# Kernel optimization log

Hardware: AMD Instinct MI355X
Metric: run time of the kernel (lower is better)

Reference implementation:

```python
import jax, jax.numpy as jnp
import numpy as np

V, DM, IMG, H, M = 32000, 256, 512, 256, 16
B, K, L, T = 16, 32, 32, 128

def setup_inputs():
    key = jax.random.key(0)
    ks = jax.random.split(key, 22)
    s = 0.02
    p = lambda i, shape: jax.random.normal(ks[i], shape, jnp.float32) * s
    return {
        "ctx_input_ids": jax.random.randint(ks[0], (B, K, L), 0, V),
        "ctx_attn_mask": jnp.ones((B, K, L), jnp.int32),
        "ctx_img_emb": jax.random.normal(ks[1], (B, K, IMG), jnp.float32),
        "tgt_input_ids": jax.random.randint(ks[2], (B, T), 0, V),
        "emb_text": p(3, (V, DM)),
        "Wih_t": p(4, (3 * DM, DM)), "Whh_t": p(5, (3 * DM, DM)),
        "bih_t": p(6, (3 * DM,)), "bhh_t": p(7, (3 * DM,)),
        "fuse_W": p(8, (H, DM + IMG)), "fuse_b": p(9, (H,)),
        "mem_init": p(10, (M, H)),
        "Wih_c": p(11, (3 * H, H)), "Whh_c": p(12, (3 * H, H)),
        "bih_c": p(13, (3 * H,)), "bhh_c": p(14, (3 * H,)),
        "tok_emb": p(15, (V, H)),
        "Wih_d": p(16, (3 * H, H)), "Whh_d": p(17, (3 * H, H)),
        "bih_d": p(18, (3 * H,)), "bhh_d": p(19, (3 * H,)),
        "head_W": p(20, (V, H)), "head_b": p(21, (V,)),
    }

def _gru(x, h0, Wih, Whh, bih, bhh, mask=None):
    # x: (B, S, I) -> outs (B, S, Hd), hN (B, Hd). PyTorch GRU equations.
    xg = jnp.einsum('bti,gi->btg', x, Wih) + bih  # precompute input-side gates (B,S,3H)
    if mask is None:
        mask = jnp.ones(x.shape[:2], bool)
    def step(h, inp):
        xt, mt = inp  # (B,3H), (B,)
        hg = h @ Whh.T + bhh
        xr, xz, xn = jnp.split(xt, 3, -1)
        hr, hz, hn = jnp.split(hg, 3, -1)
        r = jax.nn.sigmoid(xr + hr)
        z = jax.nn.sigmoid(xz + hz)
        n = jnp.tanh(xn + r * hn)
        h_new = (1.0 - z) * n + z * h
        h = jnp.where(mt[:, None], h_new, h)  # hold state on padded steps
        return h, h
    hN, outs = jax.lax.scan(step, h0, (jnp.moveaxis(xg, 1, 0), jnp.moveaxis(mask, 1, 0)))
    return jnp.moveaxis(outs, 0, 1), hN

def _forward(ctx_input_ids, ctx_attn_mask, ctx_img_emb, tgt_input_ids,
             emb_text, Wih_t, Whh_t, bih_t, bhh_t, fuse_W, fuse_b, mem_init,
             Wih_c, Whh_c, bih_c, bhh_c, tok_emb, Wih_d, Whh_d, bih_d, bhh_d,
             head_W, head_b):
    b, k, l = ctx_input_ids.shape
    dm = emb_text.shape[1]
    h = fuse_W.shape[0]
    # FrameTextEncoder: embedding + masked GRU, final hidden per frame
    tok = emb_text[ctx_input_ids.reshape(b * k, l)]  # (BK, L, DM)
    mask = ctx_attn_mask.reshape(b * k, l).astype(bool)
    _, tvec = _gru(tok, jnp.zeros((b * k, dm), tok.dtype), Wih_t, Whh_t, bih_t, bhh_t, mask)
    tvec = tvec.reshape(b, k, dm)
    # Fuse text + image
    z = jnp.tanh(jnp.concatenate([tvec, ctx_img_emb], -1) @ fuse_W.T + fuse_b)  # (B,K,H)
    # Memory slot loop over K frames (sequential softmax read then erase/add write)
    mem0 = jnp.broadcast_to(mem_init, (b,) + mem_init.shape)
    inv_sqrt_d = 1.0 / float(np.sqrt(h))
    def mem_step(mem, q):
        w = jax.nn.softmax(jnp.einsum('bmd,bd->bm', mem, q) * inv_sqrt_d, -1)
        readout = jnp.einsum('bm,bmd->bd', w, mem)
        mem = mem * (1.0 - w[..., None]) + w[..., None] * q[:, None, :]
        return mem, q + readout
    _, z_mem = jax.lax.scan(mem_step, mem0, jnp.moveaxis(z, 1, 0))
    z2 = jnp.moveaxis(z_mem, 0, 1)  # (B, K, H)
    _, h0 = _gru(z2, jnp.zeros((b, h), z2.dtype), Wih_c, Whh_c, bih_c, bhh_c)
    # Decoder over target tokens (teacher forcing)
    x = tok_emb[tgt_input_ids[:, :-1]]  # (B, T-1, H)
    outs, _ = _gru(x, h0, Wih_d, Whh_d, bih_d, bhh_d)
    return outs @ head_W.T + head_b  # (B, T-1, V)

def reference(ctx_input_ids, ctx_attn_mask, ctx_img_emb, tgt_input_ids,
              emb_text, Wih_t, Whh_t, bih_t, bhh_t, fuse_W, fuse_b, mem_init,
              Wih_c, Whh_c, bih_c, bhh_c, tok_emb, Wih_d, Whh_d, bih_d, bhh_d,
              head_W, head_b):
    return _forward(ctx_input_ids, ctx_attn_mask, ctx_img_emb, tgt_input_ids,
                    emb_text, Wih_t, Whh_t, bih_t, bhh_t, fuse_W, fuse_b, mem_init,
                    Wih_c, Whh_c, bih_c, bhh_c, tok_emb, Wih_d, Whh_d, bih_d, bhh_d,
                    head_W, head_b)
```

## Files before the change

kernel.cpp:

```cpp
#include <hip/hip_runtime.h>
#include <hip/hip_bf16.h>

typedef __attribute__((ext_vector_type(4))) float f32x4;
typedef __attribute__((ext_vector_type(8))) short short8;
typedef __attribute__((ext_vector_type(4))) unsigned int u32x4;
typedef __attribute__((ext_vector_type(4))) unsigned short u16x4;

static __device__ __forceinline__ unsigned short f2bf(float f){
  unsigned u = __builtin_bit_cast(unsigned, f);
  u += 0x7FFFu + ((u >> 16) & 1u);
  return (unsigned short)(u >> 16);
}
static __device__ __forceinline__ float bf2f(unsigned short b){
  return __builtin_bit_cast(float, ((unsigned)b) << 16);
}
static __device__ __forceinline__ unsigned char f2e4m3(float x){
  unsigned u = __builtin_bit_cast(unsigned, x);
  unsigned s = (u >> 24) & 0x80u;
  float ax = __builtin_fabsf(x);
  if (ax < 0.015625f) {
    int q = (int)(ax * 512.f + 0.5f);
    return (unsigned char)(s | (unsigned)q);
  }
  if (ax > 448.f) return (unsigned char)(s | 0x7Eu);
  unsigned v = __builtin_bit_cast(unsigned, ax);
  v += 0x00080000u + ((v >> 20) & 1u);
  if (__builtin_bit_cast(float, v & 0xFFF00000u) > 448.f)
    return (unsigned char)(s | 0x7Eu);
  unsigned ee = ((v >> 23) & 0xFFu) - 127u + 7u;
  unsigned m = (v >> 20) & 7u;
  return (unsigned char)(s | (ee << 3) | m);
}
static __device__ __forceinline__ unsigned char h2fp8(float hx16){
#if __has_builtin(__builtin_amdgcn_cvt_pk_fp8_f32)
  int pk = __builtin_amdgcn_cvt_pk_fp8_f32(hx16, hx16, 0, false);
  return (unsigned char)(pk & 0xFF);
#else
  return f2e4m3(hx16);
#endif
}
static __device__ __forceinline__ f32x4 mfma16(short8 a, short8 b, f32x4 c){
  return __builtin_amdgcn_mfma_f32_16x16x32_bf16(a, b, c, 0, 0, 0);
}
static __device__ __forceinline__ f32x4 mfma8(long a, long b, f32x4 c){
  return __builtin_amdgcn_mfma_f32_16x16x32_fp8_fp8(a, b, c, 0, 0, 0);
}
static __device__ __forceinline__ float rcpf(float x){ return __builtin_amdgcn_rcpf(x); }
static __device__ __forceinline__ float sigf(float x){ return rcpf(1.f + __expf(-x)); }
static __device__ __forceinline__ float tanhfast(float x){
  float e = __expf(2.f*x);
  return (e - 1.f) * rcpf(e + 1.f);
}

__global__ __launch_bounds__(256) void k_cvt(
    const float* __restrict__ sh, unsigned short* __restrict__ dh,
    const float* __restrict__ s0, const float* __restrict__ s1,
    const float* __restrict__ s2, const float* __restrict__ s3,
    const float* __restrict__ s4, const float* __restrict__ s5,
    const float* __restrict__ s6,
    unsigned short* __restrict__ d0, unsigned short* __restrict__ d1,
    unsigned short* __restrict__ d2, unsigned short* __restrict__ d3,
    unsigned short* __restrict__ d4, unsigned short* __restrict__ d5,
    unsigned short* __restrict__ d6)
{
  const long NH4 = 2048000;
  const long NS4 = 49152;
  const long total = NH4 + 7*NS4;
  for (long idx = (long)blockIdx.x*blockDim.x + threadIdx.x; idx < total;
       idx += (long)gridDim.x*blockDim.x) {
    const float* s; unsigned short* d; long off;
    if (idx < NH4) { s = sh; d = dh; off = idx; }
    else {
      long r = idx - NH4; int mat = (int)(r / NS4); off = r - (long)mat*NS4;
      switch (mat) {
        case 0: s=s0; d=d0; break;  case 1: s=s1; d=d1; break;
        case 2: s=s2; d=d2; break;  case 3: s=s3; d=d3; break;
        case 4: s=s4; d=d4; break;  case 5: s=s5; d=d5; break;
        default: s=s6; d=d6; break;
      }
    }
    f32x4 v = ((const f32x4*)s)[off];
    u16x4 o2;
    o2[0]=f2bf(v[0]); o2[1]=f2bf(v[1]); o2[2]=f2bf(v[2]); o2[3]=f2bf(v[3]);
    ((u16x4*)d)[off] = o2;
  }
}

__global__ __launch_bounds__(256) void k_cvtw(
    const float* __restrict__ s0, const float* __restrict__ s1,
    const float* __restrict__ s2,
    unsigned short* __restrict__ r0, unsigned short* __restrict__ r1,
    unsigned short* __restrict__ r2,
    unsigned char* __restrict__ z0, unsigned char* __restrict__ z1,
    unsigned char* __restrict__ z2)
{
  int idx = blockIdx.x*256 + threadIdx.x;
  if (idx >= 3*24576) return;
  int mat = idx / 24576, c = idx % 24576;
  const float* s = (mat==0) ? s0 : (mat==1 ? s1 : s2);
  if (c < 8192) {
    unsigned short* d = (mat==0) ? r0 : (mat==1 ? r1 : r2);
    int w = c >> 9, rest = c & 511;
    int kb = rest >> 6, lane = rest & 63;
    int row = w*16 + (lane & 15);
    int k0  = kb*32 + (lane >> 4)*8;
    const float* sp = s + (long)row*256 + k0;
    f32x4 a = *(const f32x4*)sp;
    f32x4 b = *(const f32x4*)(sp + 4);
    short8 o;
    o[0]=(short)f2bf(a[0]); o[1]=(short)f2bf(a[1]);
    o[2]=(short)f2bf(a[2]); o[3]=(short)f2bf(a[3]);
    o[4]=(short)f2bf(b[0]); o[5]=(short)f2bf(b[1]);
    o[6]=(short)f2bf(b[2]); o[7]=(short)f2bf(b[3]);
    *(short8*)(d + (long)c*8) = o;
  } else {
    int c2 = c - 8192;
    unsigned char* d = (mat==0) ? z0 : (mat==1 ? z1 : z2);
    int w = c2 >> 10, rest = c2 & 1023;
    int g = rest >> 9, r_ = rest & 511;
    int kb = r_ >> 6, lane = r_ & 63;
    int row = (1+g)*256 + w*16 + (lane & 15);
    int k0  = kb*32 + (lane >> 4)*8;
    const float* sp = s + (long)row*256 + k0;
    f32x4 a = *(const f32x4*)sp;
    f32x4 b = *(const f32x4*)(sp + 4);
    unsigned char ob[8];
    ob[0]=f2e4m3(a[0]*16.f); ob[1]=f2e4m3(a[1]*16.f);
    ob[2]=f2e4m3(a[2]*16.f); ob[3]=f2e4m3(a[3]*16.f);
    ob[4]=f2e4m3(b[0]*16.f); ob[5]=f2e4m3(b[1]*16.f);
    ob[6]=f2e4m3(b[2]*16.f); ob[7]=f2e4m3(b[3]*16.f);
    unsigned lo = (unsigned)ob[0] | ((unsigned)ob[1]<<8) |
                  ((unsigned)ob[2]<<16) | ((unsigned)ob[3]<<24);
    unsigned hi = (unsigned)ob[4] | ((unsigned)ob[5]<<8) |
                  ((unsigned)ob[6]<<16) | ((unsigned)ob[7]<<24);
    *(unsigned*)(d + (long)c2*8)     = lo;
    *(unsigned*)(d + (long)c2*8 + 4) = hi;
  }
}

template<int TN, int TS, int EPI>
__global__ __launch_bounds__(256) void k_gemm(
    const float* __restrict__ tabA, int ldA,
    const float* __restrict__ tabB2, int ldB2, int K1,
    const int* __restrict__ ids,
    const unsigned short* __restrict__ W,
    const float* __restrict__ bias,
    int M, int Ktot,
    void* __restrict__ outp, int ldOut)
{
  const int bm = blockIdx.x, bn = blockIdx.y;
  const int tid = threadIdx.x;
  const int lane = tid & 63, w = tid >> 6;
  const int l15 = lane & 15, l4 = lane >> 4;

  const int r_g = bm*64 + w*16 + l15;
  const int r_c = (r_g < M) ? r_g : (M-1);
  long row_src;
  if (ids) { int ii = (r_c / TN) * TS + (r_c % TN); row_src = ids[ii]; }
  else row_src = r_c;

  const int kchunk = l4 * 8;
  const int ncol0 = bn*128 + l15;

  f32x4 acc[8];
  #pragma unroll
  for (int i=0;i<8;i++){ f32x4 z4 = {0.f,0.f,0.f,0.f}; acc[i]=z4; }

  const int KB = Ktot >> 5;
  for (int kb = 0; kb < KB; ++kb) {
    int k = kb*32 + kchunk;
    const float* ap;
    if (tabB2 && k >= K1) ap = tabB2 + row_src*(long)ldB2 + (k - K1);
    else                  ap = tabA  + row_src*(long)ldA  + k;
    f32x4 a0 = *(const f32x4*)ap;
    f32x4 a1 = *(const f32x4*)(ap + 4);
    short8 afr;
    afr[0]=(short)f2bf(a0[0]); afr[1]=(short)f2bf(a0[1]);
    afr[2]=(short)f2bf(a0[2]); afr[3]=(short)f2bf(a0[3]);
    afr[4]=(short)f2bf(a1[0]); afr[5]=(short)f2bf(a1[1]);
    afr[6]=(short)f2bf(a1[2]); afr[7]=(short)f2bf(a1[3]);
    #pragma unroll
    for (int ct=0; ct<8; ++ct) {
      int n = ncol0 + ct*16;
      short8 bfr = *(const short8*)(W + (long)n*Ktot + k);
      acc[ct] = mfma16(afr, bfr, acc[ct]);
    }
  }

  #pragma unroll
  for (int ct=0; ct<8; ++ct) {
    int n = ncol0 + ct*16;
    float bv = bias[n];
    #pragma unroll
    for (int q=0; q<4; ++q) {
      int rr = bm*64 + w*16 + l4*4 + q;
      if (rr < M) {
        float v = acc[ct][q] + bv;
        if (EPI == 1) ((float*)outp)[(long)rr*ldOut + n] = tanhfast(v);
        else ((unsigned short*)outp)[(long)rr*ldOut + n] = f2bf(v);
      }
    }
  }
}

__global__ __launch_bounds__(1024, 1) void k_gru(
    const unsigned short* __restrict__ WR,
    const unsigned char*  __restrict__ WZN,
    const float* __restrict__ bhh,
    const unsigned short* __restrict__ xg,
    const int* __restrict__ mask,
    const unsigned short* __restrict__ h0bf,
    float* __restrict__ hNf,
    unsigned short* __restrict__ hNbf,
    unsigned short* __restrict__ outs,
    int T)
{
  __shared__ unsigned char  Wzn[131072];
  __shared__ unsigned short hbz[9*264];
  __shared__ unsigned char  h8z[9*264];
  __shared__ float          hg[4][776];

  const int tid = threadIdx.x;
  const int w = tid >> 6, lane = tid & 63;
  const int l15 = lane & 15, l4 = lane >> 4;
  const int rowbase = blockIdx.x * 4;
  const int uw = w*16 + l15;
  const int gr = tid >> 8;
  const int gu = tid & 255;

  #pragma unroll
  for (int i=0; i<8; ++i) {
    int c = i*1024 + tid;
    *(u32x4*)&Wzn[(long)c*16] = *(const u32x4*)(WZN + (long)c*16);
  }

  short8 Br[8];
  #pragma unroll
  for (int kb=0; kb<8; ++kb)
    Br[kb] = *(const short8*)(WR + ((long)(w*8+kb)*512) + lane*8);

  const float b_r = bhh[gu], b_z = bhh[256+gu], b_n = bhh[512+gu];

  const int arow0 = (l15 < 4) ? l15     : 8;
  const int arow1 = (l15 < 4) ? 4 + l15 : 8;
  const int hbO0 = (arow0*264 + l4*8)*2;
  const int hbO1 = (arow1*264 + l4*8)*2;
  const int h8O0 =  arow0*264 + l4*8;
  const int h8O1 =  arow1*264 + l4*8;

  if (tid < 264) { hbz[8*264 + tid] = 0; h8z[8*264 + tid] = 0; }
  float h = h0bf ? bf2f(h0bf[(rowbase+gr)*256 + gu]) : 0.f;
  hbz[gr*264 + gu] = f2bf(h);
  h8z[gr*264 + gu] = h2fp8(h * 16.f);
  __syncthreads();

  const float inv256 = 0.00390625f;

  for (int t=0; t<T; ++t) {
    const int p = t & 1;

    const long xrow = (long)(rowbase + gr)*T + t;
    const unsigned short* xp = xg + xrow*768;
    const unsigned short xr_ = xp[gu];
    const unsigned short xz_ = xp[256+gu];
    const unsigned short xn_ = xp[512+gu];
    const int mok = mask ? mask[xrow] : 1;

    const int hbO = p ? hbO1 : hbO0;
    const int h8O = p ? h8O1 : h8O0;
    f32x4 aR={0.f,0.f,0.f,0.f}, aZ={0.f,0.f,0.f,0.f}, aN={0.f,0.f,0.f,0.f};
    #pragma unroll
    for (int kb=0; kb<8; ++kb) {
      short8 af = *(const short8*)((const char*)hbz + hbO + kb*64);
      long   a8 = *(const long*)((const char*)h8z + h8O + kb*32);
      aR = mfma16(af, Br[kb], aR);
      aZ = mfma8(a8, *(const long*)&Wzn[((long)((w*2+0)*8+kb)*512) + lane*8], aZ);
      aN = mfma8(a8, *(const long*)&Wzn[((long)((w*2+1)*8+kb)*512) + lane*8], aN);
    }
    if (l4 == 0) {
      #pragma unroll
      for (int q=0; q<4; ++q) {
        hg[q][uw]       = aR[q];
        hg[q][256+uw]   = aZ[q];
        hg[q][512+uw]   = aN[q];
      }
    }
    __syncthreads();

    float rr = sigf(bf2f(xr_) + hg[gr][gu] + b_r);
    float zz = sigf(bf2f(xz_) + hg[gr][256+gu]*inv256 + b_z);
    float nn = tanhfast(bf2f(xn_) + rr*(hg[gr][512+gu]*inv256 + b_n));
    float hv = nn + zz*(h - nn);
    if (!mok) hv = h;
    h = hv;
    const int wrow = (p^1)*4 + gr;
    const unsigned short hbv = f2bf(hv);
    hbz[wrow*264 + gu] = hbv;
    h8z[wrow*264 + gu] = h2fp8(hv * 16.f);
    if (outs) outs[xrow*256 + gu] = hbv;
    __syncthreads();
  }

  if (hNf)  hNf[(long)(rowbase+gr)*256 + gu] = h;
  if (hNbf) hNbf[(rowbase+gr)*256 + gu] = f2bf(h);
}

__global__ __launch_bounds__(64) void k_mem(
    const float* __restrict__ z,
    const float* __restrict__ mem_init,
    float* __restrict__ z2)
{
  const int b = blockIdx.x;
  const int lane = threadIdx.x;
  float mem[16][4];
  #pragma unroll
  for (int m=0; m<16; ++m) {
    f32x4 v = *(const f32x4*)(mem_init + m*256 + lane*4);
    mem[m][0]=v[0]; mem[m][1]=v[1]; mem[m][2]=v[2]; mem[m][3]=v[3];
  }
  for (int t=0; t<32; ++t) {
    f32x4 q = *(const f32x4*)(z + ((long)b*32 + t)*256 + lane*4);
    float s[16];
    #pragma unroll
    for (int m=0; m<16; ++m)
      s[m] = mem[m][0]*q[0] + mem[m][1]*q[1] + mem[m][2]*q[2] + mem[m][3]*q[3];
    #pragma unroll
    for (int st=1; st<64; st<<=1) {
      #pragma unroll
      for (int m=0; m<16; ++m) s[m] += __shfl_xor(s[m], st, 64);
    }
    float mx = -1e30f;
    #pragma unroll
    for (int m=0; m<16; ++m) { s[m] *= 0.0625f; mx = fmaxf(mx, s[m]); }
    float sum = 0.f;
    #pragma unroll
    for (int m=0; m<16; ++m) { s[m] = __expf(s[m]-mx); sum += s[m]; }
    float inv = rcpf(sum);
    f32x4 ro = {0.f,0.f,0.f,0.f};
    #pragma unroll
    for (int m=0; m<16; ++m) {
      float wm = s[m]*inv;
      #pragma unroll
      for (int c=0; c<4; ++c) {
        ro[c] += wm * mem[m][c];
        mem[m][c] += wm * (q[c] - mem[m][c]);
      }
    }
    f32x4 o = q + ro;
    *(f32x4*)(z2 + ((long)b*32 + t)*256 + lane*4) = o;
  }
}

__global__ __launch_bounds__(256) void k_head(
    const unsigned short* __restrict__ A,
    const unsigned short* __restrict__ Bw,
    const float* __restrict__ bias,
    float* __restrict__ out,
    int M)
{
  __shared__ unsigned short Bs[32768];
  const int bid = blockIdx.x;
  const int mt = bid % 16, nt = bid / 16;
  const int tid = threadIdx.x;
  const int lane = tid & 63, w = tid >> 6;
  const int l15 = lane & 15, l4 = lane >> 4;

  const long nbase = (long)nt * 128;
  #pragma unroll
  for (int it=0; it<16; ++it) {
    int idx = it*256 + tid;
    int rr = idx >> 5;
    int ch = idx & 31;
    int sch = ch ^ (rr & 7);
    u32x4 v = *(const u32x4*)(Bw + (nbase+rr)*256 + sch*8);
    *(u32x4*)&Bs[(long)idx*8] = v;
  }
  __syncthreads();

  const int m0 = mt*128 + w*32;
  const int arow0 = m0 + l15, arow1 = arow0 + 16;
  const int kc = l4 * 8;

  f32x4 acc[2][8];
  #pragma unroll
  for (int rt=0; rt<2; ++rt)
    #pragma unroll
    for (int ct=0; ct<8; ++ct){ f32x4 z4={0.f,0.f,0.f,0.f}; acc[rt][ct]=z4; }

  #pragma unroll
  for (int kb=0; kb<8; ++kb) {
    short8 a0 = *(const short8*)(A + (long)arow0*256 + kb*32 + kc);
    short8 a1 = *(const short8*)(A + (long)arow1*256 + kb*32 + kc);
    int c = kb*4 + l4;
    #pragma unroll
    for (int ct=0; ct<8; ++ct) {
      int n_local = ct*16 + l15;
      int sc = c ^ (n_local & 7);
      short8 bf = *(const short8*)&Bs[((long)n_local*32 + sc)*8];
      acc[0][ct] = mfma16(a0, bf, acc[0][ct]);
      acc[1][ct] = mfma16(a1, bf, acc[1][ct]);
    }
  }

  #pragma unroll
  for (int ct=0; ct<8; ++ct) {
    int n_g = nt*128 + ct*16 + l15;
    float bv = bias[n_g];
    #pragma unroll
    for (int rt=0; rt<2; ++rt) {
      #pragma unroll
      for (int q=0; q<4; ++q) {
        int r_g = m0 + rt*16 + l4*4 + q;
        if (r_g < M) out[(long)r_g*32000 + n_g] = acc[rt][ct][q] + bv;
      }
    }
  }
}

extern "C" void kernel_launch(void* const* d_in, const int* in_sizes, int n_in,
                              void* d_out, int out_size, void* d_ws, size_t ws_size,
                              hipStream_t stream)
{
  (void)in_sizes; (void)n_in; (void)out_size; (void)ws_size;
  const int*   ctx_ids  = (const int*)  d_in[0];
  const int*   ctx_mask = (const int*)  d_in[1];
  const float* img      = (const float*)d_in[2];
  const int*   tgt_ids  = (const int*)  d_in[3];
  const float* emb_text = (const float*)d_in[4];
  const float* Wih_t    = (const float*)d_in[5];
  const float* Whh_t    = (const float*)d_in[6];
  const float* bih_t    = (const float*)d_in[7];
  const float* bhh_t    = (const float*)d_in[8];
  const float* fuse_W   = (const float*)d_in[9];
  const float* fuse_b   = (const float*)d_in[10];
  const float* mem_init = (const float*)d_in[11];
  const float* Wih_c    = (const float*)d_in[12];
  const float* Whh_c    = (const float*)d_in[13];
  const float* bih_c    = (const float*)d_in[14];
  const float* bhh_c    = (const float*)d_in[15];
  const float* tok_emb  = (const float*)d_in[16];
  const float* Wih_d    = (const float*)d_in[17];
  const float* Whh_d    = (const float*)d_in[18];
  const float* bih_d    = (const float*)d_in[19];
  const float* bhh_d    = (const float*)d_in[20];
  const float* head_W   = (const float*)d_in[21];
  const float* head_b   = (const float*)d_in[22];
  float* out = (float*)d_out;
  char* ws = (char*)d_ws;

  size_t o = 0;
  auto alloc = [&](size_t bytes){ size_t r = o; o += (bytes + 255) & ~(size_t)255; return r; };
  unsigned short* wWih_t = (unsigned short*)(ws + alloc(768*256*2));
  unsigned short* wWhh_t = (unsigned short*)(ws + alloc(768*256*2));
  unsigned short* wWih_c = (unsigned short*)(ws + alloc(768*256*2));
  unsigned short* wWhh_c = (unsigned short*)(ws + alloc(768*256*2));
  unsigned short* wWih_d = (unsigned short*)(ws + alloc(768*256*2));
  unsigned short* wWhh_d = (unsigned short*)(ws + alloc(768*256*2));
  unsigned short* wFuse  = (unsigned short*)(ws + alloc(256*768*2));
  unsigned short* wR_t   = (unsigned short*)(ws + alloc(65536*2));
  unsigned short* wR_c   = (unsigned short*)(ws + alloc(65536*2));
  unsigned short* wR_d   = (unsigned short*)(ws + alloc(65536*2));
  unsigned char*  wZN_t  = (unsigned char*)(ws + alloc(131072));
  unsigned char*  wZN_c  = (unsigned char*)(ws + alloc(131072));
  unsigned char*  wZN_d  = (unsigned char*)(ws + alloc(131072));
  unsigned short* wHead  = (unsigned short*)(ws + alloc((size_t)32000*256*2));
  unsigned short* xg_t   = (unsigned short*)(ws + alloc((size_t)16384*768*2));
  unsigned short* xg_c   = (unsigned short*)(ws + alloc((size_t)512*768*2));
  unsigned short* xg_d   = (unsigned short*)(ws + alloc((size_t)2032*768*2));
  float*          tvec   = (float*)(ws + alloc((size_t)512*256*4));
  float*          zbuf   = (float*)(ws + alloc((size_t)512*256*4));
  float*          z2buf  = (float*)(ws + alloc((size_t)512*256*4));
  unsigned short* outsb  = (unsigned short*)(ws + alloc((size_t)2048*256*2));
  unsigned short* hbdec  = (unsigned short*)(ws + alloc((size_t)16*256*2));

  k_cvt<<<2048, 256, 0, stream>>>(head_W, wHead,
      Wih_t, Whh_t, Wih_c, Whh_c, Wih_d, Whh_d, fuse_W,
      wWih_t, wWhh_t, wWih_c, wWhh_c, wWih_d, wWhh_d, wFuse);
  k_cvtw<<<288, 256, 0, stream>>>(Whh_t, Whh_c, Whh_d,
                                  wR_t, wR_c, wR_d, wZN_t, wZN_c, wZN_d);

  k_gemm<32,32,0><<<dim3(256,6), 256, 0, stream>>>(
      emb_text, 256, nullptr, 0, 256, ctx_ids, wWih_t, bih_t, 16384, 256, xg_t, 768);

  k_gemm<127,128,0><<<dim3(32,6), 256, 0, stream>>>(
      tok_emb, 256, nullptr, 0, 256, tgt_ids, wWih_d, bih_d, 2032, 256, xg_d, 768);

  k_gru<<<128, 1024, 0, stream>>>(wR_t, wZN_t, bhh_t, xg_t, ctx_mask,
                                  nullptr, tvec, nullptr, nullptr, 32);

  k_gemm<1,1,1><<<dim3(8,2), 256, 0, stream>>>(
      tvec, 256, img, 512, 256, nullptr, wFuse, fuse_b, 512, 768, zbuf, 256);

  k_mem<<<16, 64, 0, stream>>>(zbuf, mem_init, z2buf);

  k_gemm<1,1,0><<<dim3(8,6), 256, 0, stream>>>(
      z2buf, 256, nullptr, 0, 256, nullptr, wWih_c, bih_c, 512, 256, xg_c, 768);

  k_gru<<<4, 1024, 0, stream>>>(wR_c, wZN_c, bhh_c, xg_c, nullptr,
                                nullptr, nullptr, hbdec, nullptr, 32);

  k_gru<<<4, 1024, 0, stream>>>(wR_d, wZN_d, bhh_d, xg_d, nullptr,
                                hbdec, nullptr, nullptr, outsb, 127);

  k_head<<<4000, 256, 0, stream>>>(outsb, wHead, head_b, out, 2032);
}
```

Baseline: 728.0 us.

## Keep GRU recurrent weights in registers and redistribute gates via shuffles

The GRU step kernel no longer stages the fp8 z/n recurrent weights in shared memory; each wave keeps its slice in registers. The hidden-gate results are redistributed from the MFMA accumulator layout to per-thread units with wave shuffles instead of a shared-memory scratch buffer, which removes one block-wide barrier per timestep. Thread-to-(row,unit) mapping changes so each lane's gate values match its shuffled accumulator entries. This raises register pressure per thread and adds shuffle instructions in exchange for fewer barriers and less LDS traffic on the serial recurrence.

```diff
diff --git a/kernel.cpp b/kernel.cpp
--- a/kernel.cpp
+++ b/kernel.cpp
@@ -50,6 +50,15 @@
 static __device__ __forceinline__ float tanhfast(float x){
   float e = __expf(2.f*x);
   return (e - 1.f) * rcpf(e + 1.f);
+}
+static __device__ __forceinline__ float spread4(f32x4 v, int l15, int l4){
+  float x0 = __shfl(v[0], l15, 64);
+  float x1 = __shfl(v[1], l15, 64);
+  float x2 = __shfl(v[2], l15, 64);
+  float x3 = __shfl(v[3], l15, 64);
+  float s01 = (l4 & 1) ? x1 : x0;
+  float s23 = (l4 & 1) ? x3 : x2;
+  return (l4 & 2) ? s23 : s01;
 }
 
 __global__ __launch_bounds__(256) void k_cvt(
@@ -215,31 +224,26 @@
     unsigned short* __restrict__ outs,
     int T)
 {
-  __shared__ unsigned char  Wzn[131072];
   __shared__ unsigned short hbz[9*264];
   __shared__ unsigned char  h8z[9*264];
-  __shared__ float          hg[4][776];
 
   const int tid = threadIdx.x;
   const int w = tid >> 6, lane = tid & 63;
   const int l15 = lane & 15, l4 = lane >> 4;
   const int rowbase = blockIdx.x * 4;
-  const int uw = w*16 + l15;
-  const int gr = tid >> 8;
-  const int gu = tid & 255;
-
-  #pragma unroll
-  for (int i=0; i<8; ++i) {
-    int c = i*1024 + tid;
-    *(u32x4*)&Wzn[(long)c*16] = *(const u32x4*)(WZN + (long)c*16);
-  }
+  const int u = w*16 + l15;
+  const int gr = l4;
 
   short8 Br[8];
-  #pragma unroll
-  for (int kb=0; kb<8; ++kb)
-    Br[kb] = *(const short8*)(WR + ((long)(w*8+kb)*512) + lane*8);
-
-  const float b_r = bhh[gu], b_z = bhh[256+gu], b_n = bhh[512+gu];
+  long Bz8[8], Bn8[8];
+  #pragma unroll
+  for (int kb=0; kb<8; ++kb) {
+    Br[kb]  = *(const short8*)(WR + ((long)(w*8+kb)*512) + lane*8);
+    Bz8[kb] = *(const long*)(WZN + ((long)((w*2+0)*8+kb)*512) + lane*8);
+    Bn8[kb] = *(const long*)(WZN + ((long)((w*2+1)*8+kb)*512) + lane*8);
+  }
+
+  const float b_r = bhh[u], b_z = bhh[256+u], b_n = bhh[512+u];
 
   const int arow0 = (l15 < 4) ? l15     : 8;
   const int arow1 = (l15 < 4) ? 4 + l15 : 8;
@@ -249,9 +253,9 @@
   const int h8O1 =  arow1*264 + l4*8;
 
   if (tid < 264) { hbz[8*264 + tid] = 0; h8z[8*264 + tid] = 0; }
-  float h = h0bf ? bf2f(h0bf[(rowbase+gr)*256 + gu]) : 0.f;
-  hbz[gr*264 + gu] = f2bf(h);
-  h8z[gr*264 + gu] = h2fp8(h * 16.f);
+  float h = h0bf ? bf2f(h0bf[(rowbase+gr)*256 + u]) : 0.f;
+  hbz[gr*264 + u] = f2bf(h);
+  h8z[gr*264 + u] = h2fp8(h * 16.f);
   __syncthreads();
 
   const float inv256 = 0.00390625f;
@@ -261,9 +265,9 @@
 
     const long xrow = (long)(rowbase + gr)*T + t;
     const unsigned short* xp = xg + xrow*768;
-    const unsigned short xr_ = xp[gu];
-    const unsigned short xz_ = xp[256+gu];
-    const unsigned short xn_ = xp[512+gu];
+    const unsigned short xr_ = xp[u];
+    const unsigned short xz_ = xp[256+u];
+    const unsigned short xn_ = xp[512+u];
     const int mok = mask ? mask[xrow] : 1;
 
     const int hbO = p ? hbO1 : hbO0;
@@ -274,35 +278,30 @@
       short8 af = *(const short8*)((const char*)hbz + hbO + kb*64);
       long   a8 = *(const long*)((const char*)h8z + h8O + kb*32);
       aR = mfma16(af, Br[kb], aR);
-      aZ = mfma8(a8, *(const long*)&Wzn[((long)((w*2+0)*8+kb)*512) + lane*8], aZ);
-      aN = mfma8(a8, *(const long*)&Wzn[((long)((w*2+1)*8+kb)*512) + lane*8], aN);
-    }
-    if (l4 == 0) {
-      #pragma unroll
-      for (int q=0; q<4; ++q) {
-        hg[q][uw]       = aR[q];
-        hg[q][256+uw]   = aZ[q];
-        hg[q][512+uw]   = aN[q];
-      }
-    }
-    __syncthreads();
-
-    float rr = sigf(bf2f(xr_) + hg[gr][gu] + b_r);
-    float zz = sigf(bf2f(xz_) + hg[gr][256+gu]*inv256 + b_z);
-    float nn = tanhfast(bf2f(xn_) + rr*(hg[gr][512+gu]*inv256 + b_n));
+      aZ = mfma8(a8, Bz8[kb], aZ);
+      aN = mfma8(a8, Bn8[kb], aN);
+    }
+
+    float gR = spread4(aR, l15, l4);
+    float gZ = spread4(aZ, l15, l4);
+    float gN = spread4(aN, l15, l4);
+
+    float rr = sigf(bf2f(xr_) + gR + b_r);
+    float zz = sigf(bf2f(xz_) + gZ*inv256 + b_z);
+    float nn = tanhfast(bf2f(xn_) + rr*(gN*inv256 + b_n));
     float hv = nn + zz*(h - nn);
     if (!mok) hv = h;
     h = hv;
     const int wrow = (p^1)*4 + gr;
     const unsigned short hbv = f2bf(hv);
-    hbz[wrow*264 + gu] = hbv;
-    h8z[wrow*264 + gu] = h2fp8(hv * 16.f);
-    if (outs) outs[xrow*256 + gu] = hbv;
+    hbz[wrow*264 + u] = hbv;
+    h8z[wrow*264 + u] = h2fp8(hv * 16.f);
+    if (outs) outs[xrow*256 + u] = hbv;
     __syncthreads();
   }
 
-  if (hNf)  hNf[(long)(rowbase+gr)*256 + gu] = h;
-  if (hNbf) hNbf[(rowbase+gr)*256 + gu] = f2bf(h);
+  if (hNf)  hNf[(long)(rowbase+gr)*256 + u] = h;
+  if (hNbf) hNbf[(rowbase+gr)*256 + u] = f2bf(h);
 }
 
 __global__ __launch_bounds__(64) void k_mem(
```

Measured after the change: 670.8 us. 1.09x faster.
